# Kernel tuning notes

Hardware: AMD Instinct MI355X
Metric: run time of the kernel (lower is better)

## Reference

```python
import jax, jax.numpy as jnp
import numpy as np

B, T, D = 64, 2048, 512
UNITS = 512


def setup_inputs() -> dict:
    key = jax.random.key(0)
    ks = jax.random.split(key, 8)
    s = 1.0 / np.sqrt(D)
    return {
        "decoder_hidden": jax.random.normal(ks[0], (B, D), dtype=jnp.float32),
        "encoder_output": jax.random.normal(ks[1], (B, T, D), dtype=jnp.float32),
        "W1": jax.random.normal(ks[2], (D, UNITS), dtype=jnp.float32) * s,
        "b1": jnp.zeros((UNITS,), dtype=jnp.float32),
        "W2": jax.random.normal(ks[3], (D, UNITS), dtype=jnp.float32) * s,
        "b2": jnp.zeros((UNITS,), dtype=jnp.float32),
        "V": jax.random.normal(ks[4], (UNITS, 1), dtype=jnp.float32) * (1.0 / np.sqrt(UNITS)),
        "bV": jnp.zeros((1,), dtype=jnp.float32),
    }


def reference(decoder_hidden, encoder_output, W1, b1, W2, b2, V, bV):
    # query projection: [B, 1, U]
    q = (decoder_hidden @ W1 + b1)[:, None, :]
    # key projection: [B, T, U]
    k = jnp.einsum('btd,du->btu', encoder_output, W2) + b2
    score = jnp.tanh(q + k)                       # [B, T, U]
    logits = score @ V + bV                       # [B, T, 1]
    attention_weights = jax.nn.softmax(logits, axis=1)  # [B, T, 1]
    context_vector = jnp.sum(attention_weights * encoder_output, axis=1)  # [B, D]
    return context_vector, attention_weights
```

## Files before the change

kernel.cpp:

```cpp
#include <hip/hip_runtime.h>
#include <stdint.h>

constexpr int NB = 64;
constexpr int NT = 2048;
constexpr int ND = 512;
constexpr int NU = 512;

typedef float f32x4 __attribute__((ext_vector_type(4)));
typedef short bf16x8 __attribute__((ext_vector_type(8)));

__device__ __forceinline__ unsigned short f2bf(float x) {
  union { float f; unsigned int u; } v; v.f = x;
  unsigned int r = v.u + 0x7FFFu + ((v.u >> 16) & 1u);
  return (unsigned short)(r >> 16);
}

__device__ __forceinline__ float fast_tanh(float x) {
  return 1.0f - 2.0f / (__expf(2.0f * x) + 1.0f);
}

__global__ __launch_bounds__(512) void qproj_kernel(
    const float* __restrict__ dh, const float* __restrict__ W1,
    const float* __restrict__ b1, const float* __restrict__ b2,
    float* __restrict__ q) {
  int b = blockIdx.x;
  int u = threadIdx.x;
  const float* dr = dh + b * ND;
  float a0 = 0.f, a1 = 0.f, a2 = 0.f, a3 = 0.f;
  for (int k = 0; k < ND; k += 4) {
    a0 = fmaf(dr[k + 0], W1[(size_t)(k + 0) * NU + u], a0);
    a1 = fmaf(dr[k + 1], W1[(size_t)(k + 1) * NU + u], a1);
    a2 = fmaf(dr[k + 2], W1[(size_t)(k + 2) * NU + u], a2);
    a3 = fmaf(dr[k + 3], W1[(size_t)(k + 3) * NU + u], a3);
  }
  q[b * NU + u] = b1[u] + b2[u] + ((a0 + a1) + (a2 + a3));
}

__global__ __launch_bounds__(256) void packW2_kernel(
    const float* __restrict__ W2, unsigned short* __restrict__ w2p) {
  int tid = blockIdx.x * 256 + threadIdx.x;
  int ks = tid >> 11;
  int rem = tid & 2047;
  int ntg = rem >> 6;
  int lane = rem & 63;
  int col = ntg * 16 + (lane & 15);
  int k0 = ks * 32 + ((lane >> 4) << 3);
  const float* src = W2 + (size_t)k0 * NU + col;
  ushort4 lo, hi;
  lo.x = f2bf(src[0 * NU]); lo.y = f2bf(src[1 * NU]);
  lo.z = f2bf(src[2 * NU]); lo.w = f2bf(src[3 * NU]);
  hi.x = f2bf(src[4 * NU]); hi.y = f2bf(src[5 * NU]);
  hi.z = f2bf(src[6 * NU]); hi.w = f2bf(src[7 * NU]);
  ushort4* dst = (ushort4*)(w2p + (size_t)tid * 8);
  dst[0] = lo; dst[1] = hi;
}

__global__ __launch_bounds__(512, 4) void logits_kernel(
    const float* __restrict__ enc, const unsigned short* __restrict__ w2p,
    const float* __restrict__ q, const float* __restrict__ Vw,
    float* __restrict__ logits) {
  __shared__ unsigned short encA[64 * 512];
  __shared__ float red[8][64];

  const int tid = threadIdx.x;
  const int wave = tid >> 6;
  const int lane = tid & 63;
  const int wg = blockIdx.x;
  const int b = wg >> 5;
  const int tch = wg & 31;

  const float4* encBase = (const float4*)(enc + ((size_t)b * NT + (size_t)tch * 64) * ND);

#pragma unroll
  for (int i = 0; i < 16; ++i) {
    int idx4 = i * 512 + tid;
    int row = idx4 >> 7;
    int c4 = idx4 & 127;
    float4 v = encBase[idx4];
    ushort4 h;
    h.x = f2bf(v.x); h.y = f2bf(v.y); h.z = f2bf(v.z); h.w = f2bf(v.w);
    int byteoff = row * 1024 + ((c4 * 8) ^ ((row & 7) << 4));
    *(ushort4*)((char*)encA + byteoff) = h;
  }

  float qv[4], Vv[4];
#pragma unroll
  for (int nt = 0; nt < 4; ++nt) {
    int col = wave * 64 + nt * 16 + (lane & 15);
    qv[nt] = q[b * NU + col];
    Vv[nt] = Vw[col];
  }

  f32x4 acc[4][4];
#pragma unroll
  for (int mt = 0; mt < 4; ++mt)
#pragma unroll
    for (int nt = 0; nt < 4; ++nt)
      acc[mt][nt] = (f32x4){0.0f, 0.0f, 0.0f, 0.0f};

  const int kgrp = (lane >> 4) << 4;
  int arowbase[4], aswz[4];
#pragma unroll
  for (int mt = 0; mt < 4; ++mt) {
    int row = mt * 16 + (lane & 15);
    arowbase[mt] = row * 1024;
    aswz[mt] = (row & 7) << 4;
  }

  const char* bbase = (const char*)w2p + (size_t)(wave * 4) * 1024 + (size_t)lane * 16;

  bf16x8 bcu[4];
#pragma unroll
  for (int nt = 0; nt < 4; ++nt)
    bcu[nt] = *(const bf16x8*)(bbase + nt * 1024);

  __syncthreads();

#pragma unroll
  for (int ks = 0; ks < 16; ++ks) {
    bf16x8 bnx[4];
    if (ks < 15) {
#pragma unroll
      for (int nt = 0; nt < 4; ++nt)
        bnx[nt] = *(const bf16x8*)(bbase + (ks + 1) * 32768 + nt * 1024);
    }
    bf16x8 afr[4];
#pragma unroll
    for (int mt = 0; mt < 4; ++mt) {
      int coff = (ks * 64 + kgrp) ^ aswz[mt];
      afr[mt] = *(const bf16x8*)((const char*)encA + arowbase[mt] + coff);
    }
    __builtin_amdgcn_s_setprio(1);
#pragma unroll
    for (int mt = 0; mt < 4; ++mt)
#pragma unroll
      for (int nt = 0; nt < 4; ++nt)
        acc[mt][nt] = __builtin_amdgcn_mfma_f32_16x16x32_bf16(afr[mt], bcu[nt], acc[mt][nt], 0, 0, 0);
    __builtin_amdgcn_s_setprio(0);
    if (ks < 15) {
#pragma unroll
      for (int nt = 0; nt < 4; ++nt) bcu[nt] = bnx[nt];
    }
  }

#pragma unroll
  for (int mt = 0; mt < 4; ++mt) {
    float s0 = 0.f, s1 = 0.f, s2 = 0.f, s3 = 0.f;
#pragma unroll
    for (int nt = 0; nt < 4; ++nt) {
      s0 += fast_tanh(acc[mt][nt][0] + qv[nt]) * Vv[nt];
      s1 += fast_tanh(acc[mt][nt][1] + qv[nt]) * Vv[nt];
      s2 += fast_tanh(acc[mt][nt][2] + qv[nt]) * Vv[nt];
      s3 += fast_tanh(acc[mt][nt][3] + qv[nt]) * Vv[nt];
    }
    float sr[4] = {s0, s1, s2, s3};
#pragma unroll
    for (int r = 0; r < 4; ++r) {
      float v = sr[r];
      v += __shfl_xor(v, 1);
      v += __shfl_xor(v, 2);
      v += __shfl_xor(v, 4);
      v += __shfl_xor(v, 8);
      if ((lane & 15) == 0) red[wave][mt * 16 + ((lane >> 4) << 2) + r] = v;
    }
  }
  __syncthreads();
  if (tid < 64) {
    float t = 0.f;
#pragma unroll
    for (int w = 0; w < 8; ++w) t += red[w][tid];
    logits[(size_t)b * NT + (size_t)tch * 64 + tid] = t;
  }
}

__global__ __launch_bounds__(512) void softmax_kernel(float* __restrict__ wts) {
  int b = blockIdx.x;
  int tid = threadIdx.x;
  float4* base = (float4*)(wts + (size_t)b * NT);
  float4 v = base[tid];
  float m = fmaxf(fmaxf(v.x, v.y), fmaxf(v.z, v.w));
#pragma unroll
  for (int d = 1; d < 64; d <<= 1) m = fmaxf(m, __shfl_xor(m, d));
  __shared__ float sm[8];
  __shared__ float ss[8];
  int w = tid >> 6;
  if ((tid & 63) == 0) sm[w] = m;
  __syncthreads();
  float M = sm[0];
#pragma unroll
  for (int i = 1; i < 8; ++i) M = fmaxf(M, sm[i]);
  float e0 = __expf(v.x - M), e1 = __expf(v.y - M), e2 = __expf(v.z - M), e3 = __expf(v.w - M);
  float s = e0 + e1 + e2 + e3;
#pragma unroll
  for (int d = 1; d < 64; d <<= 1) s += __shfl_xor(s, d);
  if ((tid & 63) == 0) ss[w] = s;
  __syncthreads();
  float S = 0.f;
#pragma unroll
  for (int i = 0; i < 8; ++i) S += ss[i];
  float inv = 1.0f / S;
  base[tid] = (float4){e0 * inv, e1 * inv, e2 * inv, e3 * inv};
}

__global__ __launch_bounds__(512) void ctx_partial_kernel(
    const float* __restrict__ enc, const float* __restrict__ wts,
    float* __restrict__ partials) {
  int bx = blockIdx.x;
  int b = bx >> 4;
  int slice = bx & 15;
  int tid = threadIdx.x;
  const float* e = enc + ((size_t)b * NT + (size_t)slice * 128) * ND + tid;
  const float* wp = wts + (size_t)b * NT + slice * 128;
  float acc = 0.0f;
#pragma unroll 4
  for (int tt = 0; tt < 128; ++tt) {
    acc = fmaf(wp[tt], e[(size_t)tt * ND], acc);
  }
  partials[(size_t)bx * ND + tid] = acc;
}

__global__ __launch_bounds__(512) void ctx_combine_kernel(
    const float* __restrict__ partials, float* __restrict__ ctx) {
  int b = blockIdx.x;
  int tid = threadIdx.x;
  float s = 0.0f;
#pragma unroll
  for (int i = 0; i < 16; ++i) s += partials[((size_t)b * 16 + i) * ND + tid];
  ctx[(size_t)b * ND + tid] = s;
}

extern "C" void kernel_launch(void* const* d_in, const int* in_sizes, int n_in,
                              void* d_out, int out_size, void* d_ws, size_t ws_size,
                              hipStream_t stream) {
  const float* dh  = (const float*)d_in[0];
  const float* enc = (const float*)d_in[1];
  const float* W1  = (const float*)d_in[2];
  const float* b1  = (const float*)d_in[3];
  const float* W2  = (const float*)d_in[4];
  const float* b2  = (const float*)d_in[5];
  const float* Vw  = (const float*)d_in[6];

  float* q            = (float*)d_ws;
  unsigned short* w2p = (unsigned short*)((char*)d_ws + 131072);
  float* partials     = (float*)((char*)d_ws + 655360);

  float* ctx = (float*)d_out;
  float* wts = (float*)d_out + NB * ND;

  qproj_kernel<<<NB, 512, 0, stream>>>(dh, W1, b1, b2, q);
  packW2_kernel<<<128, 256, 0, stream>>>(W2, w2p);
  logits_kernel<<<NB * (NT / 64), 512, 0, stream>>>(enc, w2p, q, Vw, wts);
  softmax_kernel<<<NB, 512, 0, stream>>>(wts);
  ctx_partial_kernel<<<NB * 16, 512, 0, stream>>>(enc, wts, partials);
  ctx_combine_kernel<<<NB, 512, 0, stream>>>(partials, ctx);
}
```

Before: 171.2 us.

## Switch logits GEMM to 32x32x16 MFMA with repacked W2 and packed bf16 conversion

Replaces the 16x16x32 bf16 MFMA tiling in the logits kernel with 32x32x16 MFMAs (2x2 tiles of 32x32 per wave). W2 is repacked to match the new B-fragment layout, and B fragments are prefetched before the encoder tile is staged. Encoder staging now uses the hardware v_cvt_pk_bf16_f32 instruction and 16-byte LDS stores. The epilogue reduction is adapted to the 32-wide output layout. The aim is fewer MFMA issues and fewer LDS reads per FLOP. The trade-off is more shuffle steps in the epilogue and different register pressure.

```diff
diff --git a/kernel.cpp b/kernel.cpp
--- a/kernel.cpp
+++ b/kernel.cpp
@@ -7,6 +7,7 @@
 constexpr int NU = 512;
 
 typedef float f32x4 __attribute__((ext_vector_type(4)));
+typedef float f32x16 __attribute__((ext_vector_type(16)));
 typedef short bf16x8 __attribute__((ext_vector_type(8)));
 
 __device__ __forceinline__ unsigned short f2bf(float x) {
@@ -39,12 +40,11 @@
 __global__ __launch_bounds__(256) void packW2_kernel(
     const float* __restrict__ W2, unsigned short* __restrict__ w2p) {
   int tid = blockIdx.x * 256 + threadIdx.x;
-  int ks = tid >> 11;
-  int rem = tid & 2047;
-  int ntg = rem >> 6;
-  int lane = rem & 63;
-  int col = ntg * 16 + (lane & 15);
-  int k0 = ks * 32 + ((lane >> 4) << 3);
+  int lane = tid & 63;
+  int ntg = (tid >> 6) & 15;
+  int ks = tid >> 10;
+  int col = ntg * 32 + (lane & 31);
+  int k0 = ks * 16 + ((lane >> 5) << 3);
   const float* src = W2 + (size_t)k0 * NU + col;
   ushort4 lo, hi;
   lo.x = f2bf(src[0 * NU]); lo.y = f2bf(src[1 * NU]);
@@ -69,99 +69,93 @@
   const int b = wg >> 5;
   const int tch = wg & 31;
 
+  const char* bbase = (const char*)w2p + (size_t)(((2 * wave) * 64 + lane)) * 16;
+
+  bf16x8 b0a = *(const bf16x8*)(bbase);
+  bf16x8 b0b = *(const bf16x8*)(bbase + 1024);
+  bf16x8 b1a = *(const bf16x8*)(bbase + 16384);
+  bf16x8 b1b = *(const bf16x8*)(bbase + 16384 + 1024);
+
   const float4* encBase = (const float4*)(enc + ((size_t)b * NT + (size_t)tch * 64) * ND);
-
-#pragma unroll
-  for (int i = 0; i < 16; ++i) {
-    int idx4 = i * 512 + tid;
-    int row = idx4 >> 7;
-    int c4 = idx4 & 127;
-    float4 v = encBase[idx4];
-    ushort4 h;
-    h.x = f2bf(v.x); h.y = f2bf(v.y); h.z = f2bf(v.z); h.w = f2bf(v.w);
-    int byteoff = row * 1024 + ((c4 * 8) ^ ((row & 7) << 4));
-    *(ushort4*)((char*)encA + byteoff) = h;
-  }
-
-  float qv[4], Vv[4];
-#pragma unroll
-  for (int nt = 0; nt < 4; ++nt) {
-    int col = wave * 64 + nt * 16 + (lane & 15);
-    qv[nt] = q[b * NU + col];
-    Vv[nt] = Vw[col];
-  }
-
-  f32x4 acc[4][4];
-#pragma unroll
-  for (int mt = 0; mt < 4; ++mt)
-#pragma unroll
-    for (int nt = 0; nt < 4; ++nt)
-      acc[mt][nt] = (f32x4){0.0f, 0.0f, 0.0f, 0.0f};
-
-  const int kgrp = (lane >> 4) << 4;
-  int arowbase[4], aswz[4];
-#pragma unroll
-  for (int mt = 0; mt < 4; ++mt) {
-    int row = mt * 16 + (lane & 15);
-    arowbase[mt] = row * 1024;
-    aswz[mt] = (row & 7) << 4;
-  }
-
-  const char* bbase = (const char*)w2p + (size_t)(wave * 4) * 1024 + (size_t)lane * 16;
-
-  bf16x8 bcu[4];
-#pragma unroll
-  for (int nt = 0; nt < 4; ++nt)
-    bcu[nt] = *(const bf16x8*)(bbase + nt * 1024);
-
-  __syncthreads();
-
-#pragma unroll
-  for (int ks = 0; ks < 16; ++ks) {
-    bf16x8 bnx[4];
-    if (ks < 15) {
-#pragma unroll
-      for (int nt = 0; nt < 4; ++nt)
-        bnx[nt] = *(const bf16x8*)(bbase + (ks + 1) * 32768 + nt * 1024);
+#pragma unroll 4
+  for (int i = 0; i < 8; ++i) {
+    int idx8 = i * 512 + tid;
+    int row = idx8 >> 6;
+    int c8 = idx8 & 63;
+    float4 v0 = encBase[idx8 * 2];
+    float4 v1 = encBase[idx8 * 2 + 1];
+    unsigned int p0, p1, p2, p3;
+    asm("v_cvt_pk_bf16_f32 %0, %1, %2" : "=v"(p0) : "v"(v0.x), "v"(v0.y));
+    asm("v_cvt_pk_bf16_f32 %0, %1, %2" : "=v"(p1) : "v"(v0.z), "v"(v0.w));
+    asm("v_cvt_pk_bf16_f32 %0, %1, %2" : "=v"(p2) : "v"(v1.x), "v"(v1.y));
+    asm("v_cvt_pk_bf16_f32 %0, %1, %2" : "=v"(p3) : "v"(v1.z), "v"(v1.w));
+    uint4 pk; pk.x = p0; pk.y = p1; pk.z = p2; pk.w = p3;
+    int byteoff = row * 1024 + ((c8 * 16) ^ ((row & 7) << 4));
+    *(uint4*)((char*)encA + byteoff) = pk;
+  }
+
+  f32x16 acc00 = {}, acc01 = {}, acc10 = {}, acc11 = {};
+
+  const int arow0 = (lane & 31) * 1024;
+  const int arow1 = arow0 + 32 * 1024;
+  const int aswz = ((lane & 31) & 7) << 4;
+  const int kfix = (lane >> 5) << 4;
+
+  __syncthreads();
+
+#pragma unroll
+  for (int ks = 0; ks < 32; ks += 2) {
+    int ka = (ks * 32 + kfix) ^ aswz;
+    bf16x8 a0 = *(const bf16x8*)((const char*)encA + arow0 + ka);
+    bf16x8 a1 = *(const bf16x8*)((const char*)encA + arow1 + ka);
+    __builtin_amdgcn_s_setprio(1);
+    acc00 = __builtin_amdgcn_mfma_f32_32x32x16_bf16(a0, b0a, acc00, 0, 0, 0);
+    acc01 = __builtin_amdgcn_mfma_f32_32x32x16_bf16(a0, b0b, acc01, 0, 0, 0);
+    acc10 = __builtin_amdgcn_mfma_f32_32x32x16_bf16(a1, b0a, acc10, 0, 0, 0);
+    acc11 = __builtin_amdgcn_mfma_f32_32x32x16_bf16(a1, b0b, acc11, 0, 0, 0);
+    __builtin_amdgcn_s_setprio(0);
+    if (ks + 2 < 32) {
+      b0a = *(const bf16x8*)(bbase + (ks + 2) * 16384);
+      b0b = *(const bf16x8*)(bbase + (ks + 2) * 16384 + 1024);
     }
-    bf16x8 afr[4];
-#pragma unroll
-    for (int mt = 0; mt < 4; ++mt) {
-      int coff = (ks * 64 + kgrp) ^ aswz[mt];
-      afr[mt] = *(const bf16x8*)((const char*)encA + arowbase[mt] + coff);
+    int kb = ((ks + 1) * 32 + kfix) ^ aswz;
+    bf16x8 a2 = *(const bf16x8*)((const char*)encA + arow0 + kb);
+    bf16x8 a3 = *(const bf16x8*)((const char*)encA + arow1 + kb);
+    __builtin_amdgcn_s_setprio(1);
+    acc00 = __builtin_amdgcn_mfma_f32_32x32x16_bf16(a2, b1a, acc00, 0, 0, 0);
+    acc01 = __builtin_amdgcn_mfma_f32_32x32x16_bf16(a2, b1b, acc01, 0, 0, 0);
+    acc10 = __builtin_amdgcn_mfma_f32_32x32x16_bf16(a3, b1a, acc10, 0, 0, 0);
+    acc11 = __builtin_amdgcn_mfma_f32_32x32x16_bf16(a3, b1b, acc11, 0, 0, 0);
+    __builtin_amdgcn_s_setprio(0);
+    if (ks + 3 < 32) {
+      b1a = *(const bf16x8*)(bbase + (ks + 3) * 16384);
+      b1b = *(const bf16x8*)(bbase + (ks + 3) * 16384 + 1024);
     }
-    __builtin_amdgcn_s_setprio(1);
-#pragma unroll
-    for (int mt = 0; mt < 4; ++mt)
-#pragma unroll
-      for (int nt = 0; nt < 4; ++nt)
-        acc[mt][nt] = __builtin_amdgcn_mfma_f32_16x16x32_bf16(afr[mt], bcu[nt], acc[mt][nt], 0, 0, 0);
-    __builtin_amdgcn_s_setprio(0);
-    if (ks < 15) {
-#pragma unroll
-      for (int nt = 0; nt < 4; ++nt) bcu[nt] = bnx[nt];
-    }
-  }
-
-#pragma unroll
-  for (int mt = 0; mt < 4; ++mt) {
-    float s0 = 0.f, s1 = 0.f, s2 = 0.f, s3 = 0.f;
-#pragma unroll
-    for (int nt = 0; nt < 4; ++nt) {
-      s0 += fast_tanh(acc[mt][nt][0] + qv[nt]) * Vv[nt];
-      s1 += fast_tanh(acc[mt][nt][1] + qv[nt]) * Vv[nt];
-      s2 += fast_tanh(acc[mt][nt][2] + qv[nt]) * Vv[nt];
-      s3 += fast_tanh(acc[mt][nt][3] + qv[nt]) * Vv[nt];
-    }
-    float sr[4] = {s0, s1, s2, s3};
-#pragma unroll
-    for (int r = 0; r < 4; ++r) {
-      float v = sr[r];
-      v += __shfl_xor(v, 1);
-      v += __shfl_xor(v, 2);
-      v += __shfl_xor(v, 4);
-      v += __shfl_xor(v, 8);
-      if ((lane & 15) == 0) red[wave][mt * 16 + ((lane >> 4) << 2) + r] = v;
+  }
+
+  const int col = lane & 31;
+  const float qv0 = q[b * NU + wave * 64 + col];
+  const float qv1 = q[b * NU + wave * 64 + 32 + col];
+  const float Vv0 = Vw[wave * 64 + col];
+  const float Vv1 = Vw[wave * 64 + 32 + col];
+  const int hi4 = (lane >> 5) << 2;
+
+#pragma unroll
+  for (int amt = 0; amt < 2; ++amt) {
+#pragma unroll
+    for (int reg = 0; reg < 16; ++reg) {
+      float c0 = amt ? acc10[reg] : acc00[reg];
+      float c1 = amt ? acc11[reg] : acc01[reg];
+      float s = fast_tanh(c0 + qv0) * Vv0 + fast_tanh(c1 + qv1) * Vv1;
+      s += __shfl_xor(s, 1);
+      s += __shfl_xor(s, 2);
+      s += __shfl_xor(s, 4);
+      s += __shfl_xor(s, 8);
+      s += __shfl_xor(s, 16);
+      if (col == 0) {
+        int row = (reg & 3) + ((reg >> 2) << 3) + hi4;
+        red[wave][amt * 32 + row] = s;
+      }
     }
   }
   __syncthreads();
```

Measured after the change: 181.4 us. +5.9%, slower.
